# Performance work log

Measured on AMD Instinct MI355X. Metric: run time of the kernel, lower is better.

## Reference

```python
import jax, jax.numpy as jnp
import numpy as np

DIM = 512
NUM_GROUPS = 32
EPS = 1e-6
INV_SQRT2 = 0.7071067811865476


def group_norm(x, gamma, beta):
    # x: [b, c, h, w]; GroupNorm with NUM_GROUPS groups, per-channel affine
    b, c, h, w = x.shape
    xg = x.reshape(b, NUM_GROUPS, c // NUM_GROUPS, h, w)
    mu = xg.mean(axis=(2, 3, 4), keepdims=True)
    var = xg.var(axis=(2, 3, 4), keepdims=True)
    xn = ((xg - mu) * jax.lax.rsqrt(var + EPS)).reshape(b, c, h, w)
    return xn * gamma[None, :, None, None] + beta[None, :, None, None]


def conv1x1(x, w, b):
    # 1x1 conv == per-pixel GEMM over channels. w: [out_c, in_c], b: [out_c]
    return jnp.einsum('oc,bchw->bohw', w, x) + b[None, :, None, None]


def setup_inputs() -> dict:
    key = jax.random.key(0)
    ks = jax.random.split(key, 6)
    b, c, h, w = 4, DIM, 64, 64
    q = jax.random.normal(ks[0], (b, c, h, w), dtype=jnp.float32)
    init = lambda k: jax.random.normal(k, (DIM, DIM), dtype=jnp.float32) * 0.02
    return {
        'q': q,
        'gamma': jnp.ones((DIM,), jnp.float32),
        'beta': jnp.zeros((DIM,), jnp.float32),
        'wq': init(ks[1]), 'bq': jnp.zeros((DIM,), jnp.float32),
        'wk': init(ks[2]), 'bk': jnp.zeros((DIM,), jnp.float32),
        'wv': init(ks[3]), 'bv': jnp.zeros((DIM,), jnp.float32),
        'wo': init(ks[4]), 'bo': jnp.zeros((DIM,), jnp.float32),
    }


def reference(q, gamma, beta, wq, bq, wk, bk, wv, bv, wo, bo):
    q_in = q
    x = group_norm(q, gamma, beta)  # self-attention path: v is None -> v = normed q
    qp = conv1x1(x, wq, bq)
    kp = conv1x1(x, wk, bk)
    vp = conv1x1(x, wv, bv)
    b, c, h, w = qp.shape
    qf = qp.reshape(b, c, h * w)
    kf = kp.reshape(b, c, h * w)
    vf = vp.reshape(b, c, h * w)
    # scores[b, i, j] = sum_c k[b,c,i] * q[b,c,j]; softmax over i (key axis, dim=-2)
    scores = jnp.einsum('bci,bcj->bij', kf, qf) * (c ** -0.5)
    attn = jax.nn.softmax(scores, axis=-2)
    out = jnp.einsum('bci,bij->bcj', vf, attn).reshape(b, c, h, w)
    out = conv1x1(out, wo, bo)
    return (out + q_in) * INV_SQRT2
```

## Files before the change

kernel.cpp:

```cpp
#include <hip/hip_runtime.h>

typedef __bf16 bf16;
typedef __bf16 bf16x8 __attribute__((ext_vector_type(8)));
typedef float floatx4 __attribute__((ext_vector_type(4)));
typedef float floatx16 __attribute__((ext_vector_type(16)));

#define SCALE_QK 0.044194173824159216f
#define INV_SQRT2F 0.7071067811865476f
#define TEN  8388608L
#define SBAT 2097152L

typedef const __attribute__((address_space(1))) void GV;
typedef __attribute__((address_space(3))) void SV;

__global__ __launch_bounds__(256) void detect_k(
    const unsigned* __restrict__ q, int* __restrict__ flag)
{
    __shared__ int cnt;
    if (threadIdx.x == 0) cnt = 0;
    __syncthreads();
    int c = 0;
    for (int i = threadIdx.x; i < 4096; i += 256) {
        unsigned e = (q[i] >> 7) & 0xFFu;
        c += (e >= 100u && e <= 140u) ? 1 : 0;
    }
    atomicAdd(&cnt, c);
    __syncthreads();
    if (threadIdx.x == 0) *flag = (cnt < 3000) ? 1 : 0;
}

__global__ __launch_bounds__(256) void convw_k(
    const void* w0, const void* w1, const void* w2, const void* w3,
    bf16* __restrict__ dst, const int* __restrict__ flag)
{
    const void* srcs[4] = {w0, w1, w2, w3};
    const void* s = srcs[blockIdx.y];
    bf16* d = dst + (size_t)blockIdx.y * 262144;
    const int i = (blockIdx.x * 256 + threadIdx.x) * 8;
    bf16x8 v;
    if (*flag) {
        const float* f = (const float*)s;
        #pragma unroll
        for (int r = 0; r < 8; ++r) v[r] = (bf16)f[i + r];
    } else {
        v = *(const bf16x8*)((const bf16*)s + i);
    }
    *(bf16x8*)(d + i) = v;
}

__global__ __launch_bounds__(256) void convp_k(
    const void* p0, const void* p1, const void* p2,
    const void* p3, const void* p4, const void* p5,
    float* __restrict__ dst, const int* __restrict__ flag)
{
    const void* srcs[6] = {p0, p1, p2, p3, p4, p5};
    const int f = *flag;
    for (int i = threadIdx.x; i < 3072; i += 256) {
        const void* s = srcs[i >> 9];
        const int off = i & 511;
        dst[i] = f ? ((const float*)s)[off] : (float)((const bf16*)s)[off];
    }
}

__global__ __launch_bounds__(256) void groupnorm_k(
    const void* __restrict__ qraw, const float* __restrict__ gamma,
    const float* __restrict__ beta, bf16* __restrict__ XN,
    const int* __restrict__ flag)
{
    const int tid = threadIdx.x;
    const int b = blockIdx.x >> 5, g = blockIdx.x & 31;
    const int f32 = *flag;
    const size_t base = ((size_t)b * 512 + (size_t)g * 16) * 4096;
    const float* sf = (const float*)qraw + base;
    const bf16*  sb = (const bf16*)qraw + base;

    float sum = 0.f, sq = 0.f;
    if (f32) {
        const floatx4* v4 = (const floatx4*)sf;
        for (int idx = tid; idx < 16384; idx += 256) {
            floatx4 v = v4[idx];
            #pragma unroll
            for (int r = 0; r < 4; ++r) { float f = v[r]; sum += f; sq += f * f; }
        }
    } else {
        const bf16x8* v8 = (const bf16x8*)sb;
        for (int idx = tid; idx < 8192; idx += 256) {
            bf16x8 v = v8[idx];
            #pragma unroll
            for (int r = 0; r < 8; ++r) { float f = (float)v[r]; sum += f; sq += f * f; }
        }
    }
    #pragma unroll
    for (int off = 32; off; off >>= 1) {
        sum += __shfl_down(sum, off);
        sq  += __shfl_down(sq, off);
    }
    __shared__ float sS[4], sQ[4];
    __shared__ float s_mean, s_rstd;
    const int wave = tid >> 6, lane = tid & 63;
    if (lane == 0) { sS[wave] = sum; sQ[wave] = sq; }
    __syncthreads();
    if (tid == 0) {
        float ts = sS[0] + sS[1] + sS[2] + sS[3];
        float tq = sQ[0] + sQ[1] + sQ[2] + sQ[3];
        float mean = ts * (1.0f / 65536.0f);
        float var  = tq * (1.0f / 65536.0f) - mean * mean;
        s_mean = mean;
        s_rstd = rsqrtf(fmaxf(var, 0.f) + 1e-6f);
    }
    __syncthreads();
    const float mean = s_mean, rstd = s_rstd;

    float ga[16], be[16];
    #pragma unroll
    for (int c = 0; c < 16; ++c) {
        ga[c] = gamma[g * 16 + c] * rstd;
        be[c] = beta[g * 16 + c] - mean * ga[c];
    }
    bf16* dst = XN + (size_t)b * SBAT + (size_t)g * 16;
    for (int p0 = 0; p0 < 4096; p0 += 256) {
        const int p = p0 + tid;
        bf16x8 o0, o1;
        #pragma unroll
        for (int c = 0; c < 8; ++c) {
            float v = f32 ? sf[(size_t)c * 4096 + p] : (float)sb[(size_t)c * 4096 + p];
            o0[c] = (bf16)(v * ga[c] + be[c]);
        }
        #pragma unroll
        for (int c = 0; c < 8; ++c) {
            float v = f32 ? sf[(size_t)(c + 8) * 4096 + p] : (float)sb[(size_t)(c + 8) * 4096 + p];
            o1[c] = (bf16)(v * ga[c + 8] + be[c + 8]);
        }
        bf16* dp = dst + (size_t)p * 512;
        *(bf16x8*)dp = o0;
        *(bf16x8*)(dp + 8) = o1;
    }
}

__global__ __launch_bounds__(512, 2) void fused_attn(
    const bf16* __restrict__ QKt,
    const bf16* __restrict__ V,
    bf16* __restrict__ AOt)
{
    __shared__ __align__(16) char smc[147456];

    const int tid = threadIdx.x;
    const int w = tid >> 6, lane = tid & 63;
    const int fr = lane & 15, quad = lane >> 4;
    const int l5 = lane >> 5, l31 = lane & 31;

    const int ll = blockIdx.x;
    const int xcd = ll & 7, rr = ll >> 3;
    const int b = xcd >> 1;
    const int mtile = (xcd & 1) * 32 + rr;
    const int j0 = mtile * 64;

    const bf16* Qb = QKt + (size_t)b * 4194304;
    const bf16* Kb = Qb + 512;
    const bf16* Vb = V + (size_t)b * SBAT;

    const int wmQ = (w >> 1) * 16;
    const int wnQ = (w & 1) * 64;
    bf16x8 qf[16];
    {
        const bf16* qsrc = Qb + (size_t)(j0 + wmQ + fr) * 1024 + quad * 8;
        #pragma unroll
        for (int s = 0; s < 16; ++s) qf[s] = *(const bf16x8*)(qsrc + s * 32);
    }

    const int lcK = ((tid & 15) ^ ((tid >> 4) & 7)) << 3;
    const int rowK = tid >> 4;
    auto stageK = [&](int key0, int kd0, int buf) {
        char* d = smc + buf * 32768;
        const bf16* s0 = Kb + (size_t)(key0 + rowK) * 1024 + kd0 + lcK;
        #pragma unroll
        for (int rho = 0; rho < 4; ++rho)
            __builtin_amdgcn_global_load_lds((GV*)(s0 + (size_t)rho * 32 * 1024),
                (SV*)(d + rho * 8192 + tid * 16), 16, 0, 0);
    };
    const int lcV = ((tid & 3) ^ ((tid >> 3) & 3)) << 3;
    const int rowV = tid >> 2;
    auto stageV = [&](int i0, int buf) {
        char* d = smc + 65536 + buf * 32768;
        const bf16* s0 = Vb + (size_t)rowV * 4096 + i0 + lcV;
        #pragma unroll
        for (int rho = 0; rho < 4; ++rho)
            __builtin_amdgcn_global_load_lds((GV*)(s0 + (size_t)rho * 128 * 4096),
                (SV*)(d + rho * 8192 + tid * 16), 16, 0, 0);
    };

    const int wmP = (w >> 2) * 32;
    const int wnP = (w & 3) * 128;

    floatx16 acc_o[4] = {};
    float l_acc[4] = {};

    const int swzQK = (fr & 7) << 4;
    const int prow = wmP + l31;
    const int swzP = (prow & 7) << 4;

    stageK(0, 0, 0);
    __syncthreads();

    for (int c = 0; c < 32; ++c) {
        const int k0 = c * 128;
        floatx4 acc_s[4] = {};

        #pragma unroll
        for (int s = 0; s < 4; ++s) {
            if (s < 3)      stageK(k0, (s + 1) * 128, (s + 1) & 1);
            else            stageV(k0, 0);
            const char* kb = smc + (s & 1) * 32768;
            #pragma unroll
            for (int ks = 0; ks < 4; ++ks) {
                #pragma unroll
                for (int nf = 0; nf < 4; ++nf) {
                    const int key = wnQ + nf * 16 + fr;
                    bf16x8 bf8 = *(const bf16x8*)(kb + key * 256 +
                        ((ks * 64 + quad * 16) ^ swzQK));
                    acc_s[nf] = __builtin_amdgcn_mfma_f32_16x16x32_bf16(
                        qf[s * 4 + ks], bf8, acc_s[nf], 0, 0, 0);
                }
            }
            __syncthreads();
        }

        {
            float rs[4] = {0.f, 0.f, 0.f, 0.f};
            #pragma unroll
            for (int nf = 0; nf < 4; ++nf) {
                const int i = wnQ + nf * 16 + fr;
                #pragma unroll
                for (int r = 0; r < 4; ++r) {
                    const int j = wmQ + quad * 4 + r;
                    float e = __expf(fminf(acc_s[nf][r] * SCALE_QK, 30.f));
                    rs[r] += e;
                    *(bf16*)(smc + 131072 + j * 256 +
                             ((i * 2) ^ ((j & 7) << 4))) = (bf16)e;
                }
            }
            #pragma unroll
            for (int r = 0; r < 4; ++r) {
                float v = rs[r];
                v += __shfl_xor(v, 1);
                v += __shfl_xor(v, 2);
                v += __shfl_xor(v, 4);
                v += __shfl_xor(v, 8);
                l_acc[r] += v;
            }
        }
        __syncthreads();

        #pragma unroll
        for (int sv = 0; sv < 4; ++sv) {
            if (sv < 3)          stageV(k0 + (sv + 1) * 32, (sv + 1) & 1);
            else if (c < 31)     stageK(k0 + 128, 0, 0);
            const char* vb = smc + 65536 + (sv & 1) * 32768;
            const char* pb = smc + 131072;
            #pragma unroll
            for (int ih = 0; ih < 2; ++ih) {
                const int is = sv * 2 + ih;
                bf16x8 pa = *(const bf16x8*)(pb + prow * 256 +
                    ((is * 32 + l5 * 16) ^ swzP));
                #pragma unroll
                for (int nf = 0; nf < 4; ++nf) {
                    const int cc = wnP + nf * 32 + l31;
                    bf16x8 vb8 = *(const bf16x8*)(vb + cc * 64 +
                        ((ih * 32 + l5 * 16) ^ (((cc >> 1) & 3) << 4)));
                    acc_o[nf] = __builtin_amdgcn_mfma_f32_32x32x16_bf16(
                        pa, vb8, acc_o[nf], 0, 0, 0);
                }
            }
            __syncthreads();
        }
    }

    float* lsh = (float*)smc;
    if (fr == 0) {
        #pragma unroll
        for (int r = 0; r < 4; ++r) lsh[w * 16 + quad * 4 + r] = l_acc[r];
    }
    __syncthreads();
    float* rsh = (float*)(smc + 512);
    if (tid < 64) {
        const int wp = (tid >> 4) << 1;
        rsh[tid] = 1.0f / fmaxf(lsh[wp * 16 + (tid & 15)] +
                                lsh[(wp + 1) * 16 + (tid & 15)], 1e-30f);
    }
    __syncthreads();

    bf16* out = AOt + (size_t)b * SBAT + (size_t)j0 * 512;
    #pragma unroll
    for (int reg = 0; reg < 16; ++reg) {
        const int j = wmP + (reg & 3) + 8 * (reg >> 2) + 4 * l5;
        const float rl = rsh[j];
        #pragma unroll
        for (int nf = 0; nf < 4; ++nf) {
            const int cc = wnP + nf * 32 + l31;
            out[(size_t)j * 512 + cc] = (bf16)(acc_o[nf][reg] * rl);
        }
    }
}

template <int EPI>
__global__ __launch_bounds__(256, 4) void gemm_xyt(
    const bf16* __restrict__ Xb, const bf16* __restrict__ Yb,
    void* __restrict__ Cv, int N, int K, int lda, int ldb,
    long sX, long sY, long sC,
    const float* __restrict__ bias,
    const void* __restrict__ res, long sR,
    const int* __restrict__ flag)
{
    __shared__ __align__(16) bf16 smem[17408];

    const int tid  = threadIdx.x;
    const int wave = tid >> 6;
    const int lane = tid & 63;
    const int z = blockIdx.z;

    int bx = blockIdx.x, by = blockIdx.y;
    {
        const int gx = gridDim.x, gy = gridDim.y;
        const int o = by * gx + bx;
        const int xcd = o & 7, idx = o >> 3;
        if (gx == 8) {
            bx = xcd;
            by = idx;
        } else if (gx == 32 && gy == 4) {
            bx = (xcd & 1) * 16 + (idx & 15);
            by = xcd >> 1;
        }
    }

    const bf16* X = Xb + (long)z * sX;
    const bf16* Y = Yb + (long)z * sY;
    bf16*  Cb = (bf16*)Cv  + (long)z * sC;
    float* Cf = (float*)Cv + (long)z * sC;
    const int f32o = (EPI == 4) ? *flag : 0;

    const int m0 = by * 128, n0 = bx * 128;
    const int wm = (wave >> 1) * 64, wn = (wave & 1) * 64;
    const int fr = lane & 15, quad = lane >> 4;

    const int srow = tid >> 2;
    const int scol = (tid & 3) * 8;
    const bf16* pX = X + (size_t)(m0 + srow) * lda + scol;
    const bf16* pY = Y + (size_t)(n0 + srow) * ldb + scol;
    const size_t oX = (size_t)64 * lda, oY = (size_t)64 * ldb;
    char* const sb0 = (char*)smem;
    const int ldst = tid * 16;

    auto stage = [&](int k, int pb) {
        char* d = sb0 + pb * 16384;
        const bf16* x = pX + k * 32;
        const bf16* y = pY + k * 32;
        __builtin_amdgcn_global_load_lds((GV*)x,        (SV*)(d + ldst),         16, 0, 0);
        __builtin_amdgcn_global_load_lds((GV*)(x + oX), (SV*)(d + 4096 + ldst),  16, 0, 0);
        __builtin_amdgcn_global_load_lds((GV*)y,        (SV*)(d + 8192 + ldst),  16, 0, 0);
        __builtin_amdgcn_global_load_lds((GV*)(y + oY), (SV*)(d + 12288 + ldst), 16, 0, 0);
    };

    floatx4 acc[4][4] = {};
    const int NK = K >> 5;

    stage(0, 0);
    __syncthreads();

    for (int k = 0; k < NK; ++k) {
        const int p = k & 1;
        if (k + 1 < NK) stage(k + 1, 1 - p);
        const bf16* bA = smem + p * 8192;
        const bf16* bB = bA + 4096;
        bf16x8 af[4], bfr[4];
        #pragma unroll
        for (int i = 0; i < 4; ++i) {
            af[i]  = *(const bf16x8*)&bA[(wm + i * 16 + fr) * 32 + quad * 8];
            bfr[i] = *(const bf16x8*)&bB[(wn + i * 16 + fr) * 32 + quad * 8];
        }
        #pragma unroll
        for (int i = 0; i < 4; ++i)
            #pragma unroll
            for (int j = 0; j < 4; ++j)
                acc[i][j] = __builtin_amdgcn_mfma_f32_16x16x32_bf16(
                    af[i], bfr[j], acc[i][j], 0, 0, 0);
        __syncthreads();
    }

    #pragma unroll
    for (int i = 0; i < 4; ++i) {
        const int mg = m0 + wm + i * 16 + quad * 4;
        float bmr[4];
        if (EPI == 1 || EPI == 4) {
            #pragma unroll
            for (int r = 0; r < 4; ++r) bmr[r] = bias[mg + r];
        }
        #pragma unroll
        for (int j = 0; j < 4; ++j) {
            const int ng = n0 + wn + j * 16 + fr;
            #pragma unroll
            for (int r = 0; r < 4; ++r) {
                float v = acc[i][j][r];
                if (EPI == 0) v += bias[ng];
                if (EPI == 1) v += bmr[r];
                if (EPI == 4) v += bmr[r];
                acc[i][j][r] = v;
            }
        }
    }

    if (EPI != 4) {
        bf16* ct = smem;
        #pragma unroll
        for (int i = 0; i < 4; ++i)
            #pragma unroll
            for (int j = 0; j < 4; ++j)
                #pragma unroll
                for (int r = 0; r < 4; ++r)
                    ct[(wm + i * 16 + quad * 4 + r) * 132 + wn + j * 16 + fr] =
                        (bf16)acc[i][j][r];
        __syncthreads();
        #pragma unroll
        for (int w = 0; w < 8; ++w) {
            const int idx = w * 2048 + tid * 8;
            const int row = idx >> 7, col = idx & 127;
            bf16x8 v = *(const bf16x8*)&ct[row * 132 + col];
            *(bf16x8*)&Cb[(size_t)(m0 + row) * N + n0 + col] = v;
        }
    } else if (f32o) {
        float* ct = (float*)smem;
        const float* rres = (const float*)res + (size_t)z * sR;
        #pragma unroll
        for (int h = 0; h < 2; ++h) {
            if ((wave >> 1) == h) {
                #pragma unroll
                for (int i = 0; i < 4; ++i)
                    #pragma unroll
                    for (int j = 0; j < 4; ++j)
                        #pragma unroll
                        for (int r = 0; r < 4; ++r)
                            ct[(i * 16 + quad * 4 + r) * 132 + wn + j * 16 + fr] =
                                acc[i][j][r];
            }
            __syncthreads();
            #pragma unroll
            for (int w = 0; w < 8; ++w) {
                const int idx = (w * 256 + tid) * 4;
                const int row = idx >> 7, col = idx & 127;
                const size_t o = (size_t)(m0 + h * 64 + row) * N + n0 + col;
                floatx4 v = *(const floatx4*)&ct[row * 132 + col];
                floatx4 rv = *(const floatx4*)&rres[o];
                #pragma unroll
                for (int e = 0; e < 4; ++e) v[e] = (v[e] + rv[e]) * INV_SQRT2F;
                *(floatx4*)&Cf[o] = v;
            }
            __syncthreads();
        }
    } else {
        const bf16* resb = (const bf16*)res + (size_t)z * sR;
        #pragma unroll
        for (int i = 0; i < 4; ++i) {
            const int mg = m0 + wm + i * 16 + quad * 4;
            #pragma unroll
            for (int j = 0; j < 4; ++j) {
                const int ng = n0 + wn + j * 16 + fr;
                #pragma unroll
                for (int r = 0; r < 4; ++r) {
                    const size_t o = (size_t)(mg + r) * N + ng;
                    Cb[o] = (bf16)((acc[i][j][r] + (float)resb[o]) * INV_SQRT2F);
                }
            }
        }
    }
}

extern "C" void kernel_launch(void* const* d_in, const int* in_sizes, int n_in,
                              void* d_out, int out_size, void* d_ws, size_t ws_size,
                              hipStream_t stream)
{
    const void* q     = d_in[0];
    const void* gamma = d_in[1];
    const void* beta  = d_in[2];
    const void* wq    = d_in[3];
    const void* bq    = d_in[4];
    const void* wk    = d_in[5];
    const void* bk    = d_in[6];
    const void* wv    = d_in[7];
    const void* bv    = d_in[8];
    const void* wo    = d_in[9];
    const void* bo    = d_in[10];

    char* w = (char*)d_ws;
    int*   flag = (int*)w;   w += 16;
    float* Pf   = (float*)w; w += 6 * 512 * 4;
    bf16*  Wc   = (bf16*)w;  w += 4 * 262144 * 2;
    bf16*  XN   = (bf16*)w;  w += TEN * 2;
    bf16*  QKt  = (bf16*)w;  w += (size_t)4 * 4096 * 1024 * 2;
    bf16*  V    = (bf16*)w;  w += TEN * 2;
    bf16*  AOt  = XN;

    detect_k<<<dim3(1), 256, 0, stream>>>((const unsigned*)q, flag);
    convw_k<<<dim3(128, 4), 256, 0, stream>>>(wq, wk, wv, wo, Wc, flag);
    convp_k<<<dim3(1), 256, 0, stream>>>(gamma, beta, bq, bk, bv, bo, Pf, flag);

    groupnorm_k<<<dim3(128), 256, 0, stream>>>(q, Pf, Pf + 512, XN, flag);

    gemm_xyt<0><<<dim3(8, 32, 4), 256, 0, stream>>>(XN, Wc, QKt,
        1024, 512, 512, 512, SBAT, 0, (long)4096 * 1024, Pf + 1024,
        nullptr, 0, flag);
    gemm_xyt<1><<<dim3(32, 4, 4), 256, 0, stream>>>(Wc + 2 * 262144, XN, V,
        4096, 512, 512, 512, 0, SBAT, SBAT, Pf + 2048,
        nullptr, 0, flag);

    fused_attn<<<dim3(256), 512, 0, stream>>>(QKt, V, AOt);

    gemm_xyt<4><<<dim3(32, 4, 4), 256, 0, stream>>>(Wc + 3 * 262144, AOt, d_out,
        4096, 512, 512, 512, 0, SBAT, SBAT, Pf + 2560,
        q, SBAT, flag);
}
```

Before: 505.2 us.

## Transpose QK MFMA operands, vectorize P stores, and replace syncthreads with barrier-first pipeline

The QK^T MFMA now takes K as the A operand and Q as the B operand. Each lane therefore holds four consecutive keys for a single query, which lets the exp'd probabilities go to LDS as packed bf16x4 stores instead of scalar bf16 writes, and cuts the row-sum reduction to two shuffles. The trailing __syncthreads in each stage is replaced by an explicit vmcnt wait plus s_barrier at the start of the next stage, and s_setprio is raised around the MFMA loops. Launch bounds drop to one block per CU, so the compiler gets more register headroom at the cost of occupancy. Correctness depends on the new barrier placement still ordering the P-buffer writes against the following PV reads.

```diff
diff --git a/kernel.cpp b/kernel.cpp
--- a/kernel.cpp
+++ b/kernel.cpp
@@ -1,6 +1,7 @@
 #include <hip/hip_runtime.h>
 
 typedef __bf16 bf16;
+typedef __bf16 bf16x4 __attribute__((ext_vector_type(4)));
 typedef __bf16 bf16x8 __attribute__((ext_vector_type(8)));
 typedef float floatx4 __attribute__((ext_vector_type(4)));
 typedef float floatx16 __attribute__((ext_vector_type(16)));
@@ -137,7 +138,7 @@
     }
 }
 
-__global__ __launch_bounds__(512, 2) void fused_attn(
+__global__ __launch_bounds__(512, 1) void fused_attn(
     const bf16* __restrict__ QKt,
     const bf16* __restrict__ V,
     bf16* __restrict__ AOt)
@@ -152,18 +153,20 @@
     const int ll = blockIdx.x;
     const int xcd = ll & 7, rr = ll >> 3;
     const int b = xcd >> 1;
-    const int mtile = (xcd & 1) * 32 + rr;
-    const int j0 = mtile * 64;
+    const int j0 = ((xcd & 1) * 32 + rr) * 64;
 
     const bf16* Qb = QKt + (size_t)b * 4194304;
     const bf16* Kb = Qb + 512;
     const bf16* Vb = V + (size_t)b * SBAT;
 
-    const int wmQ = (w >> 1) * 16;
-    const int wnQ = (w & 1) * 64;
+    const int jb = w >> 1;
+    const int kb = w & 1;
+    const int wmP = (w >> 2) * 32;
+    const int wnP = (w & 3) * 128;
+
     bf16x8 qf[16];
     {
-        const bf16* qsrc = Qb + (size_t)(j0 + wmQ + fr) * 1024 + quad * 8;
+        const bf16* qsrc = Qb + (size_t)(j0 + jb * 16 + fr) * 1024 + quad * 8;
         #pragma unroll
         for (int s = 0; s < 16; ++s) qf[s] = *(const bf16x8*)(qsrc + s * 32);
     }
@@ -189,18 +192,19 @@
                 (SV*)(d + rho * 8192 + tid * 16), 16, 0, 0);
     };
 
-    const int wmP = (w >> 2) * 32;
-    const int wnP = (w & 3) * 128;
+    const int kxor = fr & 7;
+    const int kaddr0 = (kb * 64 + fr) * 256;
+    const int prow_ = jb * 16 + fr;
+    const int pxor = (prow_ & 7) << 4;
+    char* const pbase = smc + 131072 + prow_ * 256;
+
+    const int prowR = wmP + l31;
+    const int swzP = (prowR & 7) << 4;
 
     floatx16 acc_o[4] = {};
-    float l_acc[4] = {};
-
-    const int swzQK = (fr & 7) << 4;
-    const int prow = wmP + l31;
-    const int swzP = (prow & 7) << 4;
+    float l_acc = 0.f;
 
     stageK(0, 0, 0);
-    __syncthreads();
 
     for (int c = 0; c < 32; ++c) {
         const int k0 = c * 128;
@@ -208,59 +212,57 @@
 
         #pragma unroll
         for (int s = 0; s < 4; ++s) {
-            if (s < 3)      stageK(k0, (s + 1) * 128, (s + 1) & 1);
-            else            stageV(k0, 0);
-            const char* kb = smc + (s & 1) * 32768;
-            #pragma unroll
-            for (int ks = 0; ks < 4; ++ks) {
-                #pragma unroll
-                for (int nf = 0; nf < 4; ++nf) {
-                    const int key = wnQ + nf * 16 + fr;
-                    bf16x8 bf8 = *(const bf16x8*)(kb + key * 256 +
-                        ((ks * 64 + quad * 16) ^ swzQK));
-                    acc_s[nf] = __builtin_amdgcn_mfma_f32_16x16x32_bf16(
-                        qf[s * 4 + ks], bf8, acc_s[nf], 0, 0, 0);
+            asm volatile("s_waitcnt vmcnt(0)" ::: "memory");
+            __builtin_amdgcn_s_barrier();
+            if (s < 3) stageK(k0, (s + 1) * 128, (s + 1) & 1);
+            else       stageV(k0, 0);
+            const char* kbuf = smc + (s & 1) * 32768;
+            __builtin_amdgcn_s_setprio(1);
+            #pragma unroll
+            for (int ksl = 0; ksl < 4; ++ksl) {
+                #pragma unroll
+                for (int kf = 0; kf < 4; ++kf) {
+                    bf16x8 kf8 = *(const bf16x8*)(kbuf + kaddr0 + kf * 4096 +
+                        ((((ksl << 2) | quad) ^ kxor) << 4));
+                    acc_s[kf] = __builtin_amdgcn_mfma_f32_16x16x32_bf16(
+                        kf8, qf[s * 4 + ksl], acc_s[kf], 0, 0, 0);
                 }
             }
-            __syncthreads();
+            __builtin_amdgcn_s_setprio(0);
         }
 
         {
-            float rs[4] = {0.f, 0.f, 0.f, 0.f};
-            #pragma unroll
-            for (int nf = 0; nf < 4; ++nf) {
-                const int i = wnQ + nf * 16 + fr;
+            float rs = 0.f;
+            #pragma unroll
+            for (int kf = 0; kf < 4; ++kf) {
+                bf16x4 pk;
                 #pragma unroll
                 for (int r = 0; r < 4; ++r) {
-                    const int j = wmQ + quad * 4 + r;
-                    float e = __expf(fminf(acc_s[nf][r] * SCALE_QK, 30.f));
-                    rs[r] += e;
-                    *(bf16*)(smc + 131072 + j * 256 +
-                             ((i * 2) ^ ((j & 7) << 4))) = (bf16)e;
+                    float e = __expf(fminf(acc_s[kf][r] * SCALE_QK, 30.f));
+                    rs += e;
+                    pk[r] = (bf16)e;
                 }
-            }
-            #pragma unroll
-            for (int r = 0; r < 4; ++r) {
-                float v = rs[r];
-                v += __shfl_xor(v, 1);
-                v += __shfl_xor(v, 2);
-                v += __shfl_xor(v, 4);
-                v += __shfl_xor(v, 8);
-                l_acc[r] += v;
-            }
-        }
-        __syncthreads();
+                *(bf16x4*)(pbase + ((kb * 128 + kf * 32 + quad * 8) ^ pxor)) = pk;
+            }
+            rs += __shfl_xor(rs, 16);
+            rs += __shfl_xor(rs, 32);
+            l_acc += rs;
+            asm volatile("s_waitcnt lgkmcnt(0)" ::: "memory");
+        }
 
         #pragma unroll
         for (int sv = 0; sv < 4; ++sv) {
+            asm volatile("s_waitcnt vmcnt(0)" ::: "memory");
+            __builtin_amdgcn_s_barrier();
             if (sv < 3)          stageV(k0 + (sv + 1) * 32, (sv + 1) & 1);
             else if (c < 31)     stageK(k0 + 128, 0, 0);
             const char* vb = smc + 65536 + (sv & 1) * 32768;
             const char* pb = smc + 131072;
+            __builtin_amdgcn_s_setprio(1);
             #pragma unroll
             for (int ih = 0; ih < 2; ++ih) {
                 const int is = sv * 2 + ih;
-                bf16x8 pa = *(const bf16x8*)(pb + prow * 256 +
+                bf16x8 pa = *(const bf16x8*)(pb + prowR * 256 +
                     ((is * 32 + l5 * 16) ^ swzP));
                 #pragma unroll
                 for (int nf = 0; nf < 4; ++nf) {
@@ -271,21 +273,19 @@
                         pa, vb8, acc_o[nf], 0, 0, 0);
                 }
             }
-            __syncthreads();
-        }
-    }
+            __builtin_amdgcn_s_setprio(0);
+        }
+    }
+    asm volatile("s_waitcnt vmcnt(0)" ::: "memory");
+    __syncthreads();
 
     float* lsh = (float*)smc;
-    if (fr == 0) {
-        #pragma unroll
-        for (int r = 0; r < 4; ++r) lsh[w * 16 + quad * 4 + r] = l_acc[r];
-    }
+    if (lane < 16) lsh[w * 16 + lane] = l_acc;
     __syncthreads();
     float* rsh = (float*)(smc + 512);
     if (tid < 64) {
-        const int wp = (tid >> 4) << 1;
-        rsh[tid] = 1.0f / fmaxf(lsh[wp * 16 + (tid & 15)] +
-                                lsh[(wp + 1) * 16 + (tid & 15)], 1e-30f);
+        const int jbq = tid >> 4, t = tid & 15;
+        rsh[tid] = 1.0f / fmaxf(lsh[jbq * 32 + t] + lsh[jbq * 32 + 16 + t], 1e-30f);
     }
     __syncthreads();
 
```

Measured after the change: 473.4 us. 1.07x faster.
